# Optimization experiments

Measured on AMD Instinct MI355X. Metric: run time of the kernel, lower is better.

Reference implementation:

```python
import jax, jax.numpy as jnp
import numpy as np

B, N, DIM, H = 1, 768, 384, 12
SK, SV, PK, PV, PD = 16, 16, 4, 4, 128
NUM_LOGITS = 3
SCALAR_SCALE = (NUM_LOGITS * SK) ** -0.5
POINT_SCALE = (NUM_LOGITS * PK * (9.0 / 2.0)) ** -0.5
PAIR_SCALE = NUM_LOGITS ** -0.5
EPS = 1e-8
SOFTPLUS_INV_1 = float(np.log(np.e - 1.0))  # torch init: log(exp(1)-1)


def setup_inputs() -> dict:
    key = jax.random.key(0)
    ks = jax.random.split(key, 16)
    w = lambda k, shape: (jax.random.normal(k, shape, jnp.float32) * 0.02)
    return {
        "single_repr": jax.random.normal(ks[0], (B, N, DIM), jnp.float32),
        "pairwise_repr": jax.random.normal(ks[1], (B, N, N, PD), jnp.float32),
        "rotations": jax.random.normal(ks[2], (B, N, 3, 3), jnp.float32),
        "translations": jax.random.normal(ks[3], (B, N, 3), jnp.float32),
        "mask": jnp.ones((B, N), dtype=bool),
        "Wq_s": w(ks[4], (DIM, H * SK)),
        "Wk_s": w(ks[5], (DIM, H * SK)),
        "Wv_s": w(ks[6], (DIM, H * SV)),
        "Wq_p": w(ks[7], (DIM, H * PK * 3)),
        "Wk_p": w(ks[8], (DIM, H * PK * 3)),
        "Wv_p": w(ks[9], (DIM, H * PV * 3)),
        "W_pair": w(ks[10], (PD, H)),
        "b_pair": jnp.zeros((H,), jnp.float32),
        "point_weights": jnp.full((H,), SOFTPLUS_INV_1, jnp.float32),
        "W_out": w(ks[11], (H * (SV + PD + PV * 4), DIM)),
        "b_out": jnp.zeros((DIM,), jnp.float32),
    }


def _ipa(single_repr, pairwise_repr, rotations, translations, mask,
         Wq_s, Wk_s, Wv_s, Wq_p, Wk_p, Wv_p, W_pair, b_pair,
         point_weights, W_out, b_out):
    x = single_repr
    # scalar q/k/v: (b,n,h*d) -> (b,h,n,d)
    heads_s = lambda t, d: t.reshape(B, N, H, d).transpose(0, 2, 1, 3)
    q_s = heads_s(x @ Wq_s, SK)
    k_s = heads_s(x @ Wk_s, SK)
    v_s = heads_s(x @ Wv_s, SV)
    # point q/k/v: (b,n,h*d*3) -> (b,h,n,d,3), then apply global frame
    heads_p = lambda t, d: t.reshape(B, N, H, d, 3).transpose(0, 2, 1, 3, 4)
    trans = translations[:, None, :, None, :]  # (b,1,n,1,3)
    to_global = lambda t: jnp.einsum('bhndc,bnrc->bhndr', t, rotations) + trans
    q_p = to_global(heads_p(x @ Wq_p, PK))
    k_p = to_global(heads_p(x @ Wk_p, PK))
    v_p = to_global(heads_p(x @ Wv_p, PV))

    logits = jnp.einsum('bhid,bhjd->bhij', q_s, k_s) * SCALAR_SCALE
    pair_bias = pairwise_repr @ W_pair + b_pair  # (b,i,j,h)
    logits = logits + pair_bias.transpose(0, 3, 1, 2) * PAIR_SCALE
    diff = q_p[:, :, :, None] - k_p[:, :, None]  # (b,h,i,j,d,3)
    point_dist = jnp.sum(diff * diff, axis=(-2, -1))  # (b,h,i,j)
    pw = jax.nn.softplus(point_weights)[None, :, None, None]
    logits = logits - 0.5 * POINT_SCALE * pw * point_dist

    m2 = (mask[:, :, None] & mask[:, None, :])[:, None]  # (b,1,i,j)
    logits = jnp.where(m2, logits, -jnp.finfo(logits.dtype).max)
    attn = jax.nn.softmax(logits, axis=-1)

    r_scalar = jnp.einsum('bhij,bhjd->bhid', attn, v_s)
    r_pair = jnp.einsum('bhij,bijd->bhid', attn, pairwise_repr)
    r_point = jnp.einsum('bhij,bhjdc->bhidc', attn, v_p) - trans
    # back to local frame: multiply by R^T
    r_point = jnp.einsum('bhndc,bncr->bhndr', r_point, rotations)
    r_pnorm = jnp.sqrt(jnp.sum(r_point * r_point, axis=-1) + EPS)

    flat = lambda t: t.transpose(0, 2, 1, 3).reshape(B, N, -1)
    f_point = r_point.transpose(0, 2, 1, 3, 4).reshape(B, N, -1)
    results = jnp.concatenate(
        [flat(r_scalar), f_point, flat(r_pnorm), flat(r_pair)], axis=-1)
    return results @ W_out + b_out


def reference(single_repr, pairwise_repr, rotations, translations, mask,
              Wq_s, Wk_s, Wv_s, Wq_p, Wk_p, Wv_p, W_pair, b_pair,
              point_weights, W_out, b_out):
    return _ipa(single_repr, pairwise_repr, rotations, translations, mask,
                Wq_s, Wk_s, Wv_s, Wq_p, Wk_p, Wv_p, W_pair, b_pair,
                point_weights, W_out, b_out)
```

## Files before the change

kernel.cpp:

```cpp
#include <hip/hip_runtime.h>
#include <math.h>

#define NRES 768
#define DIMM 384
#define NH   12

#define SCALAR_SCALE 0.14433756729740646f
#define HALF_POINT   0.06804138174397717f
#define PAIR_SCALE   0.5773502691896258f

__global__ __launch_bounds__(256) void k1_proj(
    const float* __restrict__ x, const float* __restrict__ rot, const float* __restrict__ trans,
    const float* __restrict__ Wqs, const float* __restrict__ Wks, const float* __restrict__ Wvs,
    const float* __restrict__ Wqp, const float* __restrict__ Wkp, const float* __restrict__ Wvp,
    float* __restrict__ qs, float* __restrict__ ks, float* __restrict__ vs,
    float* __restrict__ qpg, float* __restrict__ kpg, float* __restrict__ vpg)
{
    __shared__ float xs[4 * 384];
    __shared__ float xp[3][4][144];

    const int tid = threadIdx.x;
    const int n0 = blockIdx.x * 4;

    for (int idx = tid; idx < 384; idx += 256) {
        float4 v = ((const float4*)(x + (size_t)n0 * 384))[idx];
        ((float4*)xs)[idx] = v;
    }
    __syncthreads();

    if (tid < 252) {
        const int g = tid;
        int m, c0, wd;
        if (g < 144) { m = g / 48; c0 = (g - m * 48) * 4; wd = 192; }
        else { int z = g - 144; m = 3 + z / 36; c0 = (z - (m - 3) * 36) * 4; wd = 144; }
        const float* Wm = (m==0)?Wqs : (m==1)?Wks : (m==2)?Wvs : (m==3)?Wqp : (m==4)?Wkp : Wvp;
        const float* wp = Wm + c0;
        float acc[4][4] = {};
        #pragma unroll 2
        for (int k = 0; k < DIMM; ++k) {
            float4 w = *(const float4*)wp; wp += wd;
            #pragma unroll
            for (int r = 0; r < 4; ++r) {
                float xv = xs[r * 384 + k];
                acc[r][0] = fmaf(xv, w.x, acc[r][0]);
                acc[r][1] = fmaf(xv, w.y, acc[r][1]);
                acc[r][2] = fmaf(xv, w.z, acc[r][2]);
                acc[r][3] = fmaf(xv, w.w, acc[r][3]);
            }
        }
        if (m < 3) {
            float* dst = (m==0)?qs : (m==1)?ks : vs;
            #pragma unroll
            for (int r = 0; r < 4; ++r) {
                float4 st = make_float4(acc[r][0], acc[r][1], acc[r][2], acc[r][3]);
                *(float4*)(dst + (size_t)(n0 + r) * 192 + c0) = st;
            }
        } else {
            int mi = m - 3;
            #pragma unroll
            for (int r = 0; r < 4; ++r)
                #pragma unroll
                for (int u = 0; u < 4; ++u) xp[mi][r][c0 + u] = acc[r][u];
        }
    }
    __syncthreads();

    for (int t = tid; t < 576; t += 256) {
        int mi = t / 192; int rm = t - mi * 192; int r = rm / 48; int pt = rm - r * 48; int c0 = pt * 3;
        float p0 = xp[mi][r][c0+0], p1 = xp[mi][r][c0+1], p2 = xp[mi][r][c0+2];
        int n = n0 + r;
        const float* R = rot + n * 9; const float* T = trans + n * 3;
        float g0 = fmaf(R[0], p0, fmaf(R[1], p1, fmaf(R[2], p2, T[0])));
        float g1 = fmaf(R[3], p0, fmaf(R[4], p1, fmaf(R[5], p2, T[1])));
        float g2 = fmaf(R[6], p0, fmaf(R[7], p1, fmaf(R[8], p2, T[2])));
        float* dst = (mi==0)?qpg : (mi==1)?kpg : vpg;
        dst[n*144 + c0+0] = g0; dst[n*144 + c0+1] = g1; dst[n*144 + c0+2] = g2;
    }
}

__global__ __launch_bounds__(256, 3) void k2_attn(
    const float* __restrict__ pairwise, const float* __restrict__ rot, const float* __restrict__ trans,
    const float* __restrict__ Wp, const float* __restrict__ bp, const float* __restrict__ ptw,
    const float* __restrict__ qs, const float* __restrict__ ks, const float* __restrict__ vs,
    const float* __restrict__ qpg, const float* __restrict__ kpg, const float* __restrict__ vpg,
    float* __restrict__ results)
{
    __shared__ float Pt[64 * 129];
    __shared__ float PBp[4 * 64 * 13];
    __shared__ float E[64 * 13];
    __shared__ float Qs[192], Qp[144];
    __shared__ float mL[12], lL[12], aL[12], invL[12], hpL[12], bpL[12];
    __shared__ float rp_l[144];

    const int tid = threadIdx.x;
    const int i = blockIdx.x;
    const size_t ri = (size_t)i * 1920;

    if (tid < 48)                    ((float4*)Qs)[tid]      = ((const float4*)(qs  + (size_t)i * 192))[tid];
    if (tid >= 64 && tid < 100)      ((float4*)Qp)[tid - 64] = ((const float4*)(qpg + (size_t)i * 144))[tid - 64];
    if (tid >= 128 && tid < 140) {
        int h = tid - 128;
        hpL[h] = HALF_POINT * log1pf(__expf(ptw[h]));
        bpL[h] = PAIR_SCALE * bp[h];
        mL[h] = -3.0e38f; lL[h] = 0.f;
    }
    __syncthreads();

    const int j  = tid & 63;
    const int hg = tid >> 6;
    const int hh = tid >> 7, dpr = tid & 127, hb = hh * 6;

    float accp[6] = {0.f,0.f,0.f,0.f,0.f,0.f};
    float accs = 0.f, accq = 0.f;
    const int hs = tid >> 4;
    const int hq = tid / 12;

    for (int tile = 0; tile < 12; ++tile) {
        const int j0 = tile * 64;

        {
            const float4* Pg = (const float4*)(pairwise + ((size_t)i * NRES + j0) * 128);
            #pragma unroll
            for (int q = 0; q < 8; ++q) {
                int idx = tid + 256 * q;
                float4 v = Pg[idx];
                int row = idx >> 5, c4 = (idx & 31) << 2;
                float* dp = &Pt[row * 129 + c4];
                dp[0] = v.x; dp[1] = v.y; dp[2] = v.z; dp[3] = v.w;
            }
        }
        __syncthreads();

        {
            float pbp[12];
            #pragma unroll
            for (int h = 0; h < 12; ++h) pbp[h] = 0.f;
            const int d0 = hg * 32;
            #pragma unroll 4
            for (int d = 0; d < 32; ++d) {
                float p = Pt[j * 129 + d0 + d];
                const float* w = Wp + (d0 + d) * 12;
                #pragma unroll
                for (int h = 0; h < 12; ++h) pbp[h] = fmaf(p, w[h], pbp[h]);
            }
            const int jg = j0 + j;
            const float* kr = ks  + (size_t)jg * 192;
            const float* kp = kpg + (size_t)jg * 144;
            float own[3];
            #pragma unroll
            for (int e = 0; e < 3; ++e) {
                int h = 3 * hg + e;
                const float4* kv = (const float4*)(kr + h * 16);
                float4 a0 = kv[0], a1 = kv[1], a2 = kv[2], a3 = kv[3];
                const float4* qv = (const float4*)(Qs + h * 16);
                float4 q0 = qv[0], q1 = qv[1], q2 = qv[2], q3 = qv[3];
                float s = q0.x*a0.x + q0.y*a0.y + q0.z*a0.z + q0.w*a0.w
                        + q1.x*a1.x + q1.y*a1.y + q1.z*a1.z + q1.w*a1.w
                        + q2.x*a2.x + q2.y*a2.y + q2.z*a2.z + q2.w*a2.w
                        + q3.x*a3.x + q3.y*a3.y + q3.z*a3.z + q3.w*a3.w;
                const float4* pv = (const float4*)(kp + h * 12);
                float4 p0 = pv[0], p1 = pv[1], p2 = pv[2];
                const float4* qpv = (const float4*)(Qp + h * 12);
                float4 u0 = qpv[0], u1 = qpv[1], u2 = qpv[2];
                float d0v, dist;
                d0v = u0.x - p0.x; dist  = d0v*d0v;
                d0v = u0.y - p0.y; dist += d0v*d0v;
                d0v = u0.z - p0.z; dist += d0v*d0v;
                d0v = u0.w - p0.w; dist += d0v*d0v;
                d0v = u1.x - p1.x; dist += d0v*d0v;
                d0v = u1.y - p1.y; dist += d0v*d0v;
                d0v = u1.z - p1.z; dist += d0v*d0v;
                d0v = u1.w - p1.w; dist += d0v*d0v;
                d0v = u2.x - p2.x; dist += d0v*d0v;
                d0v = u2.y - p2.y; dist += d0v*d0v;
                d0v = u2.z - p2.z; dist += d0v*d0v;
                d0v = u2.w - p2.w; dist += d0v*d0v;
                own[e] = SCALAR_SCALE * s - hpL[h] * dist + bpL[h];
            }
            float* pbw = &PBp[hg * 832 + j * 13];
            #pragma unroll
            for (int h = 0; h < 12; ++h) {
                float v = PAIR_SCALE * pbp[h];
                if (h >= 3 * hg && h < 3 * hg + 3) v += own[h - 3 * hg];
                pbw[h] = v;
            }
        }
        __syncthreads();

        {
            const float* pbr = &PBp[j * 13];
            float Lv[3], tm[3];
            #pragma unroll
            for (int e = 0; e < 3; ++e) {
                int h = 3 * hg + e;
                Lv[e] = pbr[h] + pbr[832 + h] + pbr[1664 + h] + pbr[2496 + h];
                tm[e] = Lv[e];
            }
            #pragma unroll
            for (int o = 32; o > 0; o >>= 1) {
                #pragma unroll
                for (int e = 0; e < 3; ++e) tm[e] = fmaxf(tm[e], __shfl_xor(tm[e], o));
            }
            float ss[3], mnv[3], alv[3];
            #pragma unroll
            for (int e = 0; e < 3; ++e) {
                int h = 3 * hg + e;
                float mo = mL[h];
                float mn = fmaxf(mo, tm[e]);
                alv[e] = __expf(mo - mn);
                mnv[e] = mn;
                float ev = __expf(Lv[e] - mn);
                E[j * 13 + h] = ev;
                ss[e] = ev;
            }
            #pragma unroll
            for (int o = 32; o > 0; o >>= 1) {
                #pragma unroll
                for (int e = 0; e < 3; ++e) ss[e] += __shfl_xor(ss[e], o);
            }
            if (j == 0) {
                #pragma unroll
                for (int e = 0; e < 3; ++e) {
                    int h = 3 * hg + e;
                    mL[h] = mnv[e]; aL[h] = alv[e];
                    lL[h] = lL[h] * alv[e] + ss[e];
                }
            }
        }
        __syncthreads();

        {
            #pragma unroll
            for (int u = 0; u < 6; ++u) accp[u] *= aL[hb + u];
            #pragma unroll 4
            for (int jj = 0; jj < 64; ++jj) {
                float p = Pt[jj * 129 + dpr];
                const float* ej = &E[jj * 13 + hb];
                accp[0] = fmaf(ej[0], p, accp[0]);
                accp[1] = fmaf(ej[1], p, accp[1]);
                accp[2] = fmaf(ej[2], p, accp[2]);
                accp[3] = fmaf(ej[3], p, accp[3]);
                accp[4] = fmaf(ej[4], p, accp[4]);
                accp[5] = fmaf(ej[5], p, accp[5]);
            }
        }
        if (tid < 192) {
            accs *= aL[hs];
            const float* vb = vs + (size_t)j0 * 192 + tid;
            #pragma unroll 4
            for (int jj = 0; jj < 64; ++jj)
                accs = fmaf(E[jj * 13 + hs], vb[(size_t)jj * 192], accs);
        }
        if (tid < 144) {
            accq *= aL[hq];
            const float* vb = vpg + (size_t)j0 * 144 + tid;
            #pragma unroll 4
            for (int jj = 0; jj < 64; ++jj)
                accq = fmaf(E[jj * 13 + hq], vb[(size_t)jj * 144], accq);
        }
        __syncthreads();
    }

    if (tid < 12) invL[tid] = 1.0f / lL[tid];
    __syncthreads();

    #pragma unroll
    for (int u = 0; u < 6; ++u)
        results[ri + 384 + (size_t)(hb + u) * 128 + dpr] = accp[u] * invL[hb + u];

    if (tid < 192) results[ri + tid] = accs * invL[hs];

    if (tid < 144) {
        int pc = tid - hq * 12;
        int coord = pc - (pc / 3) * 3;
        rp_l[tid] = accq * invL[hq] - trans[i * 3 + coord];
    }
    __syncthreads();

    if (tid < 48) {
        int h = tid >> 2, d = tid & 3; int c0 = h * 12 + d * 3;
        float p0 = rp_l[c0], p1 = rp_l[c0 + 1], p2 = rp_l[c0 + 2];
        const float* R = rot + i * 9;
        float o0 = p0 * R[0] + p1 * R[3] + p2 * R[6];
        float o1 = p0 * R[1] + p1 * R[4] + p2 * R[7];
        float o2 = p0 * R[2] + p1 * R[5] + p2 * R[8];
        results[ri + 192 + c0 + 0] = o0;
        results[ri + 192 + c0 + 1] = o1;
        results[ri + 192 + c0 + 2] = o2;
        results[ri + 336 + h * 4 + d] = sqrtf(o0*o0 + o1*o1 + o2*o2 + 1e-8f);
    }
}

__global__ __launch_bounds__(384) void k3_out(
    const float* __restrict__ results, const float* __restrict__ Wo, const float* __restrict__ bo,
    float* __restrict__ out)
{
    __shared__ float As[4 * 1924];
    __shared__ float red[3 * 96 * 17];

    const int t = threadIdx.x;
    const int r0 = blockIdx.x * 4;

    #pragma unroll
    for (int q = 0; q < 5; ++q) {
        int idx = t + 384 * q;
        if (idx < 1920) {
            int r = idx / 480, c4 = idx - r * 480;
            float4 v = ((const float4*)(results + (size_t)(r0 + r) * 1920))[c4];
            float* dp = &As[r * 1924 + c4 * 4];
            dp[0] = v.x; dp[1] = v.y; dp[2] = v.z; dp[3] = v.w;
        }
    }
    __syncthreads();

    const int cg = t % 96, kp = t / 96;
    float acc[4][4] = {};
    const float* wp = Wo + (size_t)(kp * 480) * 384 + cg * 4;
    int ka = kp * 480;
    #pragma unroll 2
    for (int k = 0; k < 480; ++k, ++ka) {
        float4 w = *(const float4*)wp; wp += 384;
        #pragma unroll
        for (int r = 0; r < 4; ++r) {
            float a = As[r * 1924 + ka];
            acc[r][0] = fmaf(a, w.x, acc[r][0]);
            acc[r][1] = fmaf(a, w.y, acc[r][1]);
            acc[r][2] = fmaf(a, w.z, acc[r][2]);
            acc[r][3] = fmaf(a, w.w, acc[r][3]);
        }
    }
    if (kp > 0) {
        float* rp = &red[((kp - 1) * 96 + cg) * 17];
        #pragma unroll
        for (int r = 0; r < 4; ++r)
            #pragma unroll
            for (int u = 0; u < 4; ++u) rp[r * 4 + u] = acc[r][u];
    }
    __syncthreads();
    if (kp == 0) {
        float4 b = *(const float4*)(bo + cg * 4);
        #pragma unroll
        for (int r = 0; r < 4; ++r) {
            const float* r1 = &red[(0 * 96 + cg) * 17 + r * 4];
            const float* r2 = &red[(1 * 96 + cg) * 17 + r * 4];
            const float* r3 = &red[(2 * 96 + cg) * 17 + r * 4];
            float4 o;
            o.x = acc[r][0] + r1[0] + r2[0] + r3[0] + b.x;
            o.y = acc[r][1] + r1[1] + r2[1] + r3[1] + b.y;
            o.z = acc[r][2] + r1[2] + r2[2] + r3[2] + b.z;
            o.w = acc[r][3] + r1[3] + r2[3] + r3[3] + b.w;
            *(float4*)(out + (size_t)(r0 + r) * 384 + cg * 4) = o;
        }
    }
}

extern "C" void kernel_launch(void* const* d_in, const int* in_sizes, int n_in,
                              void* d_out, int out_size, void* d_ws, size_t ws_size,
                              hipStream_t stream) {
    const float* x        = (const float*)d_in[0];
    const float* pairwise = (const float*)d_in[1];
    const float* rot      = (const float*)d_in[2];
    const float* trans    = (const float*)d_in[3];
    const float* Wqs   = (const float*)d_in[5];
    const float* Wks   = (const float*)d_in[6];
    const float* Wvs   = (const float*)d_in[7];
    const float* Wqp   = (const float*)d_in[8];
    const float* Wkp   = (const float*)d_in[9];
    const float* Wvp   = (const float*)d_in[10];
    const float* Wp    = (const float*)d_in[11];
    const float* bp    = (const float*)d_in[12];
    const float* ptw   = (const float*)d_in[13];
    const float* Wo    = (const float*)d_in[14];
    const float* bo    = (const float*)d_in[15];
    float* out = (float*)d_out;

    float* ws = (float*)d_ws;
    float* qs      = ws;
    float* ksb     = qs   + 147456;
    float* vsb     = ksb  + 147456;
    float* qpg     = vsb  + 147456;
    float* kpg     = qpg  + 110592;
    float* vpg     = kpg  + 110592;
    float* results = vpg  + 110592;

    hipLaunchKernelGGL(k1_proj, dim3(192), dim3(256), 0, stream,
                       x, rot, trans, Wqs, Wks, Wvs, Wqp, Wkp, Wvp,
                       qs, ksb, vsb, qpg, kpg, vpg);
    hipLaunchKernelGGL(k2_attn, dim3(768), dim3(256), 0, stream,
                       pairwise, rot, trans, Wp, bp, ptw,
                       qs, ksb, vsb, qpg, kpg, vpg, results);
    hipLaunchKernelGGL(k3_out, dim3(192), dim3(384), 0, stream,
                       results, Wo, bo, out);
}
```

Before: 877.9 us.

## Prefetch pairwise tiles into registers, drop pair-bias reduction, halve rows per block

In the attention kernel, the next 64-row tile of the pairwise tensor is prefetched into registers while the current one is processed. The pair-bias projection is restructured so each thread computes all 128 dims for its 3 heads, which removes the PBp shared buffer and one barrier per tile. Occupancy hint goes from 3 to 4 blocks, the E stride is padded to allow float2 reads, and the projection and output kernels process 2 rows per block instead of 4 so more blocks launch. The costs are extra register pressure from the prefetch buffer and redundant Wp reads per thread.

```diff
diff --git a/kernel.cpp b/kernel.cpp
--- a/kernel.cpp
+++ b/kernel.cpp
@@ -16,16 +16,14 @@
     float* __restrict__ qs, float* __restrict__ ks, float* __restrict__ vs,
     float* __restrict__ qpg, float* __restrict__ kpg, float* __restrict__ vpg)
 {
-    __shared__ float xs[4 * 384];
-    __shared__ float xp[3][4][144];
+    __shared__ float xs[2 * 384];
+    __shared__ float xp[3][2][144];
 
     const int tid = threadIdx.x;
-    const int n0 = blockIdx.x * 4;
-
-    for (int idx = tid; idx < 384; idx += 256) {
-        float4 v = ((const float4*)(x + (size_t)n0 * 384))[idx];
-        ((float4*)xs)[idx] = v;
-    }
+    const int n0 = blockIdx.x * 2;
+
+    for (int idx = tid; idx < 192; idx += 256)
+        ((float4*)xs)[idx] = ((const float4*)(x + (size_t)n0 * 384))[idx];
     __syncthreads();
 
     if (tid < 252) {
@@ -35,12 +33,12 @@
         else { int z = g - 144; m = 3 + z / 36; c0 = (z - (m - 3) * 36) * 4; wd = 144; }
         const float* Wm = (m==0)?Wqs : (m==1)?Wks : (m==2)?Wvs : (m==3)?Wqp : (m==4)?Wkp : Wvp;
         const float* wp = Wm + c0;
-        float acc[4][4] = {};
-        #pragma unroll 2
+        float acc[2][4] = {};
+        #pragma unroll 4
         for (int k = 0; k < DIMM; ++k) {
             float4 w = *(const float4*)wp; wp += wd;
             #pragma unroll
-            for (int r = 0; r < 4; ++r) {
+            for (int r = 0; r < 2; ++r) {
                 float xv = xs[r * 384 + k];
                 acc[r][0] = fmaf(xv, w.x, acc[r][0]);
                 acc[r][1] = fmaf(xv, w.y, acc[r][1]);
@@ -51,22 +49,22 @@
         if (m < 3) {
             float* dst = (m==0)?qs : (m==1)?ks : vs;
             #pragma unroll
-            for (int r = 0; r < 4; ++r) {
+            for (int r = 0; r < 2; ++r) {
                 float4 st = make_float4(acc[r][0], acc[r][1], acc[r][2], acc[r][3]);
                 *(float4*)(dst + (size_t)(n0 + r) * 192 + c0) = st;
             }
         } else {
             int mi = m - 3;
             #pragma unroll
-            for (int r = 0; r < 4; ++r)
+            for (int r = 0; r < 2; ++r)
                 #pragma unroll
                 for (int u = 0; u < 4; ++u) xp[mi][r][c0 + u] = acc[r][u];
         }
     }
     __syncthreads();
 
-    for (int t = tid; t < 576; t += 256) {
-        int mi = t / 192; int rm = t - mi * 192; int r = rm / 48; int pt = rm - r * 48; int c0 = pt * 3;
+    for (int t = tid; t < 288; t += 256) {
+        int mi = t / 96; int rm = t - mi * 96; int r = rm / 48; int pt = rm - r * 48; int c0 = pt * 3;
         float p0 = xp[mi][r][c0+0], p1 = xp[mi][r][c0+1], p2 = xp[mi][r][c0+2];
         int n = n0 + r;
         const float* R = rot + n * 9; const float* T = trans + n * 3;
@@ -78,7 +76,7 @@
     }
 }
 
-__global__ __launch_bounds__(256, 3) void k2_attn(
+__global__ __launch_bounds__(256, 4) void k2_attn(
     const float* __restrict__ pairwise, const float* __restrict__ rot, const float* __restrict__ trans,
     const float* __restrict__ Wp, const float* __restrict__ bp, const float* __restrict__ ptw,
     const float* __restrict__ qs, const float* __restrict__ ks, const float* __restrict__ vs,
@@ -86,8 +84,7 @@
     float* __restrict__ results)
 {
     __shared__ float Pt[64 * 129];
-    __shared__ float PBp[4 * 64 * 13];
-    __shared__ float E[64 * 13];
+    __shared__ float E[64 * 14];
     __shared__ float Qs[192], Qp[144];
     __shared__ float mL[12], lL[12], aL[12], invL[12], hpL[12], bpL[12];
     __shared__ float rp_l[144];
@@ -96,56 +93,48 @@
     const int i = blockIdx.x;
     const size_t ri = (size_t)i * 1920;
 
-    if (tid < 48)                    ((float4*)Qs)[tid]      = ((const float4*)(qs  + (size_t)i * 192))[tid];
-    if (tid >= 64 && tid < 100)      ((float4*)Qp)[tid - 64] = ((const float4*)(qpg + (size_t)i * 144))[tid - 64];
+    if (tid < 48)               ((float4*)Qs)[tid]      = ((const float4*)(qs  + (size_t)i * 192))[tid];
+    if (tid >= 64 && tid < 100) ((float4*)Qp)[tid - 64] = ((const float4*)(qpg + (size_t)i * 144))[tid - 64];
     if (tid >= 128 && tid < 140) {
         int h = tid - 128;
         hpL[h] = HALF_POINT * log1pf(__expf(ptw[h]));
         bpL[h] = PAIR_SCALE * bp[h];
         mL[h] = -3.0e38f; lL[h] = 0.f;
     }
-    __syncthreads();
 
     const int j  = tid & 63;
-    const int hg = tid >> 6;
+    const int hg = __builtin_amdgcn_readfirstlane(tid >> 6);
     const int hh = tid >> 7, dpr = tid & 127, hb = hh * 6;
+    const int hs = tid >> 4;
+    const int hq = tid / 12;
+
+    const float4* Pg = (const float4*)(pairwise + (size_t)i * NRES * 128);
+    float4 pf[8];
+    #pragma unroll
+    for (int q = 0; q < 8; ++q) pf[q] = Pg[tid + 256 * q];
 
     float accp[6] = {0.f,0.f,0.f,0.f,0.f,0.f};
     float accs = 0.f, accq = 0.f;
-    const int hs = tid >> 4;
-    const int hq = tid / 12;
 
     for (int tile = 0; tile < 12; ++tile) {
-        const int j0 = tile * 64;
+        #pragma unroll
+        for (int q = 0; q < 8; ++q) {
+            int idx = tid + 256 * q;
+            int row = idx >> 5, c4 = (idx & 31) << 2;
+            float* dp = &Pt[row * 129 + c4];
+            dp[0] = pf[q].x; dp[1] = pf[q].y; dp[2] = pf[q].z; dp[3] = pf[q].w;
+        }
+        if (tile < 11) {
+            const float4* Pn = Pg + (size_t)(tile + 1) * 2048;
+            #pragma unroll
+            for (int q = 0; q < 8; ++q) pf[q] = Pn[tid + 256 * q];
+        }
+        __syncthreads();
 
         {
-            const float4* Pg = (const float4*)(pairwise + ((size_t)i * NRES + j0) * 128);
-            #pragma unroll
-            for (int q = 0; q < 8; ++q) {
-                int idx = tid + 256 * q;
-                float4 v = Pg[idx];
-                int row = idx >> 5, c4 = (idx & 31) << 2;
-                float* dp = &Pt[row * 129 + c4];
-                dp[0] = v.x; dp[1] = v.y; dp[2] = v.z; dp[3] = v.w;
-            }
-        }
-        __syncthreads();
-
-        {
-            float pbp[12];
-            #pragma unroll
-            for (int h = 0; h < 12; ++h) pbp[h] = 0.f;
-            const int d0 = hg * 32;
-            #pragma unroll 4
-            for (int d = 0; d < 32; ++d) {
-                float p = Pt[j * 129 + d0 + d];
-                const float* w = Wp + (d0 + d) * 12;
-                #pragma unroll
-                for (int h = 0; h < 12; ++h) pbp[h] = fmaf(p, w[h], pbp[h]);
-            }
-            const int jg = j0 + j;
-            const float* kr = ks  + (size_t)jg * 192;
-            const float* kp = kpg + (size_t)jg * 144;
+            const int jg = tile * 64 + j;
+            const float* kr  = ks  + (size_t)jg * 192;
+            const float* kpr = kpg + (size_t)jg * 144;
             float own[3];
             #pragma unroll
             for (int e = 0; e < 3; ++e) {
@@ -158,44 +147,41 @@
                         + q1.x*a1.x + q1.y*a1.y + q1.z*a1.z + q1.w*a1.w
                         + q2.x*a2.x + q2.y*a2.y + q2.z*a2.z + q2.w*a2.w
                         + q3.x*a3.x + q3.y*a3.y + q3.z*a3.z + q3.w*a3.w;
-                const float4* pv = (const float4*)(kp + h * 12);
+                const float4* pv = (const float4*)(kpr + h * 12);
                 float4 p0 = pv[0], p1 = pv[1], p2 = pv[2];
                 const float4* qpv = (const float4*)(Qp + h * 12);
                 float4 u0 = qpv[0], u1 = qpv[1], u2 = qpv[2];
-                float d0v, dist;
-                d0v = u0.x - p0.x; dist  = d0v*d0v;
-                d0v = u0.y - p0.y; dist += d0v*d0v;
-                d0v = u0.z - p0.z; dist += d0v*d0v;
-                d0v = u0.w - p0.w; dist += d0v*d0v;
-                d0v = u1.x - p1.x; dist += d0v*d0v;
-                d0v = u1.y - p1.y; dist += d0v*d0v;
-                d0v = u1.z - p1.z; dist += d0v*d0v;
-                d0v = u1.w - p1.w; dist += d0v*d0v;
-                d0v = u2.x - p2.x; dist += d0v*d0v;
-                d0v = u2.y - p2.y; dist += d0v*d0v;
-                d0v = u2.z - p2.z; dist += d0v*d0v;
-                d0v = u2.w - p2.w; dist += d0v*d0v;
+                float dv, dist;
+                dv = u0.x - p0.x; dist  = dv*dv;
+                dv = u0.y - p0.y; dist += dv*dv;
+                dv = u0.z - p0.z; dist += dv*dv;
+                dv = u0.w - p0.w; dist += dv*dv;
+                dv = u1.x - p1.x; dist += dv*dv;
+                dv = u1.y - p1.y; dist += dv*dv;
+                dv = u1.z - p1.z; dist += dv*dv;
+                dv = u1.w - p1.w; dist += dv*dv;
+                dv = u2.x - p2.x; dist += dv*dv;
+                dv = u2.y - p2.y; dist += dv*dv;
+                dv = u2.z - p2.z; dist += dv*dv;
+                dv = u2.w - p2.w; dist += dv*dv;
                 own[e] = SCALAR_SCALE * s - hpL[h] * dist + bpL[h];
             }
-            float* pbw = &PBp[hg * 832 + j * 13];
-            #pragma unroll
-            for (int h = 0; h < 12; ++h) {
-                float v = PAIR_SCALE * pbp[h];
-                if (h >= 3 * hg && h < 3 * hg + 3) v += own[h - 3 * hg];
-                pbw[h] = v;
-            }
-        }
-        __syncthreads();
-
-        {
-            const float* pbr = &PBp[j * 13];
+            float pb0 = 0.f, pb1 = 0.f, pb2 = 0.f;
+            const float* Prow = &Pt[j * 129];
+            const float* Wh = Wp + 3 * hg;
+            #pragma unroll 8
+            for (int d = 0; d < 128; ++d) {
+                float p = Prow[d];
+                pb0 = fmaf(p, Wh[d * 12 + 0], pb0);
+                pb1 = fmaf(p, Wh[d * 12 + 1], pb1);
+                pb2 = fmaf(p, Wh[d * 12 + 2], pb2);
+            }
             float Lv[3], tm[3];
-            #pragma unroll
-            for (int e = 0; e < 3; ++e) {
-                int h = 3 * hg + e;
-                Lv[e] = pbr[h] + pbr[832 + h] + pbr[1664 + h] + pbr[2496 + h];
-                tm[e] = Lv[e];
-            }
+            Lv[0] = own[0] + PAIR_SCALE * pb0;
+            Lv[1] = own[1] + PAIR_SCALE * pb1;
+            Lv[2] = own[2] + PAIR_SCALE * pb2;
+            #pragma unroll
+            for (int e = 0; e < 3; ++e) tm[e] = Lv[e];
             #pragma unroll
             for (int o = 32; o > 0; o >>= 1) {
                 #pragma unroll
@@ -210,7 +196,7 @@
                 alv[e] = __expf(mo - mn);
                 mnv[e] = mn;
                 float ev = __expf(Lv[e] - mn);
-                E[j * 13 + h] = ev;
+                E[j * 14 + h] = ev;
                 ss[e] = ev;
             }
             #pragma unroll
@@ -235,28 +221,29 @@
             #pragma unroll 4
             for (int jj = 0; jj < 64; ++jj) {
                 float p = Pt[jj * 129 + dpr];
-                const float* ej = &E[jj * 13 + hb];
-                accp[0] = fmaf(ej[0], p, accp[0]);
-                accp[1] = fmaf(ej[1], p, accp[1]);
-                accp[2] = fmaf(ej[2], p, accp[2]);
-                accp[3] = fmaf(ej[3], p, accp[3]);
-                accp[4] = fmaf(ej[4], p, accp[4]);
-                accp[5] = fmaf(ej[5], p, accp[5]);
+                const float2* ej = (const float2*)&E[jj * 14 + hb];
+                float2 e01 = ej[0], e23 = ej[1], e45 = ej[2];
+                accp[0] = fmaf(e01.x, p, accp[0]);
+                accp[1] = fmaf(e01.y, p, accp[1]);
+                accp[2] = fmaf(e23.x, p, accp[2]);
+                accp[3] = fmaf(e23.y, p, accp[3]);
+                accp[4] = fmaf(e45.x, p, accp[4]);
+                accp[5] = fmaf(e45.y, p, accp[5]);
             }
         }
         if (tid < 192) {
             accs *= aL[hs];
-            const float* vb = vs + (size_t)j0 * 192 + tid;
+            const float* vb = vs + (size_t)tile * 64 * 192 + tid;
             #pragma unroll 4
             for (int jj = 0; jj < 64; ++jj)
-                accs = fmaf(E[jj * 13 + hs], vb[(size_t)jj * 192], accs);
+                accs = fmaf(E[jj * 14 + hs], vb[(size_t)jj * 192], accs);
         }
         if (tid < 144) {
             accq *= aL[hq];
-            const float* vb = vpg + (size_t)j0 * 144 + tid;
+            const float* vb = vpg + (size_t)tile * 64 * 144 + tid;
             #pragma unroll 4
             for (int jj = 0; jj < 64; ++jj)
-                accq = fmaf(E[jj * 13 + hq], vb[(size_t)jj * 144], accq);
+                accq = fmaf(E[jj * 14 + hq], vb[(size_t)jj * 144], accq);
         }
         __syncthreads();
     }
@@ -295,34 +282,30 @@
     const float* __restrict__ results, const float* __restrict__ Wo, const float* __restrict__ bo,
     float* __restrict__ out)
 {
-    __shared__ float As[4 * 1924];
-    __shared__ float red[3 * 96 * 17];
+    __shared__ float As[2 * 1920];
+    __shared__ float red[3 * 96 * 9];
 
     const int t = threadIdx.x;
-    const int r0 = blockIdx.x * 4;
+    const int r0 = blockIdx.x * 2;
 
     #pragma unroll
-    for (int q = 0; q < 5; ++q) {
+    for (int q = 0; q < 3; ++q) {
         int idx = t + 384 * q;
-        if (idx < 1920) {
-            int r = idx / 480, c4 = idx - r * 480;
-            float4 v = ((const float4*)(results + (size_t)(r0 + r) * 1920))[c4];
-            float* dp = &As[r * 1924 + c4 * 4];
-            dp[0] = v.x; dp[1] = v.y; dp[2] = v.z; dp[3] = v.w;
-        }
+        if (idx < 960)
+            ((float4*)As)[idx] = ((const float4*)(results + (size_t)r0 * 1920))[idx];
     }
     __syncthreads();
 
     const int cg = t % 96, kp = t / 96;
-    float acc[4][4] = {};
+    float acc[2][4] = {};
     const float* wp = Wo + (size_t)(kp * 480) * 384 + cg * 4;
-    int ka = kp * 480;
-    #pragma unroll 2
-    for (int k = 0; k < 480; ++k, ++ka) {
+    const float* ap = As + kp * 480;
+    #pragma unroll 4
+    for (int k = 0; k < 480; ++k) {
         float4 w = *(const float4*)wp; wp += 384;
         #pragma unroll
-        for (int r = 0; r < 4; ++r) {
-            float a = As[r * 1924 + ka];
+        for (int r = 0; r < 2; ++r) {
+            float a = ap[r * 1920 + k];
             acc[r][0] = fmaf(a, w.x, acc[r][0]);
             acc[r][1] = fmaf(a, w.y, acc[r][1]);
             acc[r][2] = fmaf(a, w.z, acc[r][2]);
@@ -330,9 +313,9 @@
         }
     }
     if (kp > 0) {
-        float* rp = &red[((kp - 1) * 96 + cg) * 17];
+        float* rp = &red[((kp - 1) * 96 + cg) * 9];
         #pragma unroll
-        for (int r = 0; r < 4; ++r)
+        for (int r = 0; r < 2; ++r)
             #pragma unroll
             for (int u = 0; u < 4; ++u) rp[r * 4 + u] = acc[r][u];
     }
@@ -340,10 +323,10 @@
     if (kp == 0) {
         float4 b = *(const float4*)(bo + cg * 4);
         #pragma unroll
-        for (int r = 0; r < 4; ++r) {
-            const float* r1 = &red[(0 * 96 + cg) * 17 + r * 4];
-            const float* r2 = &red[(1 * 96 + cg) * 17 + r * 4];
-            const float* r3 = &red[(2 * 96 + cg) * 17 + r * 4];
+        for (int r = 0; r < 2; ++r) {
+            const float* r1 = &red[(0 * 96 + cg) * 9 + r * 4];
+            const float* r2 = &red[(1 * 96 + cg) * 9 + r * 4];
+            const float* r3 = &red[(2 * 96 + cg) * 9 + r * 4];
             float4 o;
             o.x = acc[r][0] + r1[0] + r2[0] + r3[0] + b.x;
             o.y = acc[r][1] + r1[1] + r2[1] + r3[1] + b.y;
@@ -383,12 +366,12 @@
     float* vpg     = kpg  + 110592;
     float* results = vpg  + 110592;
 
-    hipLaunchKernelGGL(k1_proj, dim3(192), dim3(256), 0, stream,
+    hipLaunchKernelGGL(k1_proj, dim3(384), dim3(256), 0, stream,
                        x, rot, trans, Wqs, Wks, Wvs, Wqp, Wkp, Wvp,
                        qs, ksb, vsb, qpg, kpg, vpg);
     hipLaunchKernelGGL(k2_attn, dim3(768), dim3(256), 0, stream,
                        pairwise, rot, trans, Wp, bp, ptw,
                        qs, ksb, vsb, qpg, kpg, vpg, results);
-    hipLaunchKernelGGL(k3_out, dim3(192), dim3(384), 0, stream,
+    hipLaunchKernelGGL(k3_out, dim3(384), dim3(384), 0, stream,
                        results, Wo, bo, out);
 }
```

New measurement: 1.074 ms. 1.22x slower.
